# Optimization experiments

Measured on AMD Instinct MI355X. Metric: run time of the kernel, lower is better.

Reference implementation:

```python
import jax, jax.numpy as jnp
import numpy as np

B, S, HID = 2, 4096, 2048
NH, NKV, HD = 16, 4, 128  # num_heads, num_kv_heads, head_dim
GROUPS = NH // NKV
ROPE_THETA = 10000.0


def _rope_cos_sin(position_ids):
    # position_ids: [B, S] int
    inv_freq = 1.0 / (ROPE_THETA ** (jnp.arange(0, HD, 2, dtype=jnp.float32) / HD))  # [HD/2]
    freqs = position_ids.astype(jnp.float32)[..., None] * inv_freq  # [B, S, HD/2]
    emb = jnp.concatenate([freqs, freqs], axis=-1)  # [B, S, HD]
    return jnp.cos(emb), jnp.sin(emb)


def _rotate_half(x):
    x1, x2 = jnp.split(x, 2, axis=-1)
    return jnp.concatenate([-x2, x1], axis=-1)


def _apply_rope(q, k, cos, sin):
    # q: [B, NH, S, HD], k: [B, NKV, S, HD]; cos/sin: [B, S, HD]
    cos = cos[:, None, :, :]
    sin = sin[:, None, :, :]
    q = q * cos + _rotate_half(q) * sin
    k = k * cos + _rotate_half(k) * sin
    return q, k


def kappa(x):
    return jax.nn.elu(x) + 1.0


def setup_inputs() -> dict:
    key = jax.random.key(0)
    ks = jax.random.split(key, 8)
    sc = 0.02
    hidden_states = jax.random.normal(ks[0], (B, S, HID), dtype=jnp.float32)
    position_ids = jnp.broadcast_to(jnp.arange(S, dtype=jnp.int64)[None, :], (B, S))
    Wq = jax.random.normal(ks[1], (HID, NH * HD), dtype=jnp.float32) * sc
    Wk = jax.random.normal(ks[2], (HID, NKV * HD), dtype=jnp.float32) * sc
    Wv = jax.random.normal(ks[3], (HID, NKV * HD), dtype=jnp.float32) * sc
    Wo = jax.random.normal(ks[4], (HID, HID), dtype=jnp.float32) * sc
    Wphi = jax.random.normal(ks[5], (HID, HID), dtype=jnp.float32) * sc
    bphi = jax.random.normal(ks[6], (HID,), dtype=jnp.float32) * sc
    return {"hidden_states": hidden_states, "position_ids": position_ids,
            "Wq": Wq, "Wk": Wk, "Wv": Wv, "Wo": Wo, "Wphi": Wphi, "bphi": bphi}


def reference(hidden_states, position_ids, Wq, Wk, Wv, Wo, Wphi, bphi):
    b, s, _ = hidden_states.shape
    # projections -> [B, heads, S, HD]
    q = (hidden_states @ Wq).reshape(b, s, NH, HD).transpose(0, 2, 1, 3)
    k = (hidden_states @ Wk).reshape(b, s, NKV, HD).transpose(0, 2, 1, 3)
    v = (hidden_states @ Wv).reshape(b, s, NKV, HD).transpose(0, 2, 1, 3)
    cos, sin = _rope_cos_sin(position_ids)
    q, k = _apply_rope(q, k, cos, sin)
    # GQA expand kv heads
    k = jnp.repeat(k, GROUPS, axis=1)  # [B, NH, S, HD]
    v = jnp.repeat(v, GROUPS, axis=1)
    Qk = kappa(q)
    Kk = kappa(k)
    Qg = Qk.mean(axis=2)  # [B, NH, HD]
    logits = jnp.einsum('bnd,bnsd->bns', Qg, Kk)
    alpha = jax.nn.softmax(logits, axis=-1) * float(s)  # [B, NH, S]
    outer_sum = jnp.einsum('bns,bnsd,bnsf->bndf', alpha, Kk, v)  # [B, NH, HD, HD]
    X_phi = (hidden_states @ Wphi + bphi).reshape(b, s, NH, HD).transpose(0, 2, 1, 3)
    result_attn = jnp.einsum('bnsd,bndf->bnsf', Qk, outer_sum)
    context = (X_phi * result_attn).transpose(0, 2, 1, 3).reshape(b, s, HID)
    return context @ Wo
```

## Files before the change

kernel.cpp:

```cpp
#include <hip/hip_runtime.h>
#include <hip/hip_bf16.h>
#include <math.h>

#define B_    2
#define S_    4096
#define HID_  2048
#define NH_   16
#define NKV_  4
#define HD_   128
#define GROUPS_ (NH_/NKV_)
#define ROPE_THETA_ 10000.0f
#define OSPLIT 8
#define QCH   32

typedef __attribute__((ext_vector_type(8))) short short8;
typedef __attribute__((ext_vector_type(4))) float f32x4;

__device__ inline unsigned short f2bf(float f) {
    __hip_bfloat16 h = __float2bfloat16(f);
    return *(unsigned short*)&h;
}

__device__ inline float bf2f(short u) {
    union { unsigned int i; float f; } v;
    v.i = ((unsigned int)(unsigned short)u) << 16;
    return v.f;
}

__device__ inline void gload16(const void* g, void* l) {
    __builtin_amdgcn_global_load_lds((const __attribute__((address_space(1))) void*)g,
                                     (__attribute__((address_space(3))) void*)l, 16, 0, 0);
}

#define BARM() asm volatile("s_barrier" ::: "memory")

__global__ void rope_table_kernel(float* __restrict__ cosT, float* __restrict__ sinT) {
    int s = blockIdx.x;
    int i = threadIdx.x;
    float expo = -2.0f * (float)i / (float)HD_;
    float invf = powf(ROPE_THETA_, expo);
    float f = (float)s * invf;
    cosT[s * 64 + i] = cosf(f);
    sinT[s * 64 + i] = sinf(f);
}

__global__ void cast_bf16_kernel(const float* __restrict__ in,
                                 __hip_bfloat16* __restrict__ out, int n8) {
    int i = blockIdx.x * 256 + threadIdx.x;
    if (i >= n8) return;
    const float4 v0 = *reinterpret_cast<const float4*>(&in[i * 8]);
    const float4 v1 = *reinterpret_cast<const float4*>(&in[i * 8 + 4]);
    union { short8 v; unsigned short u[8]; } o;
    o.u[0] = f2bf(v0.x); o.u[1] = f2bf(v0.y); o.u[2] = f2bf(v0.z); o.u[3] = f2bf(v0.w);
    o.u[4] = f2bf(v1.x); o.u[5] = f2bf(v1.y); o.u[6] = f2bf(v1.z); o.u[7] = f2bf(v1.w);
    *reinterpret_cast<short8*>(&out[i * 8]) = o.v;
}

__global__ __launch_bounds__(256) void transpose_cast_kernel(
        const float* __restrict__ W, __hip_bfloat16* __restrict__ Wt, int K, int N) {
    __shared__ float T[64][65];
    int k0 = blockIdx.y * 64, n0 = blockIdx.x * 64;
    int tid = threadIdx.x;
    int r = tid >> 4, c4 = (tid & 15) * 4;
#pragma unroll
    for (int p = 0; p < 4; ++p) {
        float4 v = *reinterpret_cast<const float4*>(&W[(size_t)(k0 + r + p * 16) * N + n0 + c4]);
        T[r + p * 16][c4 + 0] = v.x;
        T[r + p * 16][c4 + 1] = v.y;
        T[r + p * 16][c4 + 2] = v.z;
        T[r + p * 16][c4 + 3] = v.w;
    }
    __syncthreads();
#pragma unroll
    for (int p = 0; p < 4; ++p) {
        int n = r + p * 16;
        short4 o;
        o.x = (short)f2bf(T[c4 + 0][n]);
        o.y = (short)f2bf(T[c4 + 1][n]);
        o.z = (short)f2bf(T[c4 + 2][n]);
        o.w = (short)f2bf(T[c4 + 3][n]);
        *reinterpret_cast<short4*>(&Wt[(size_t)(n0 + n) * K + k0 + c4]) = o;
    }
}

__device__ __forceinline__ void stage_region(const __hip_bfloat16* __restrict__ src,
        int ldK, int row0, int kbase, __hip_bfloat16* dst, int tid) {
#pragma unroll
    for (int g = 0; g < 2; ++g) {
        int P = g * 512 + tid;
        int row = P >> 2, cp = P & 3;
        int cl = cp ^ ((row >> 1) & 3);
        gload16(src + (size_t)(row0 + row) * ldK + kbase + cl * 8, dst + P * 8);
    }
}

__device__ __forceinline__ void stage_region128(const __hip_bfloat16* __restrict__ src,
        int ldK, int row0, int kbase, __hip_bfloat16* dst, int tid) {
#pragma unroll
    for (int g = 0; g < 2; ++g) {
        int P = g * 256 + tid;
        int row = P >> 2, cp = P & 3;
        int cl = cp ^ ((row >> 1) & 3);
        gload16(src + (size_t)(row0 + row) * ldK + kbase + cl * 8, dst + P * 8);
    }
}

#define BM 128
#define BN 128
#define T128EL 8192
__global__ __launch_bounds__(256) void gemm_mfma_kernel(
        const __hip_bfloat16* __restrict__ A, const __hip_bfloat16* __restrict__ Bt,
        float* __restrict__ C, const float* __restrict__ bias, int M, int N, int K) {
    __shared__ __hip_bfloat16 lds[4 * T128EL];
    int tid  = threadIdx.x;
    int wid  = tid >> 6, lane = tid & 63;
    int wr   = wid >> 1, wc = wid & 1;
    int lr = lane & 15, lc = lane >> 4;
    int c16 = lc ^ ((lr >> 1) & 3);
    int bm = blockIdx.y * BM, bn = blockIdx.x * BN;

    f32x4 acc[4][4];
#pragma unroll
    for (int m = 0; m < 4; ++m)
#pragma unroll
        for (int n = 0; n < 4; ++n)
#pragma unroll
            for (int i = 0; i < 4; ++i) acc[m][n][i] = 0.0f;

    const int NKT = K >> 5;

    stage_region128(A,  K, bm, 0,  lds,                 tid);
    stage_region128(Bt, K, bn, 0,  lds + 4096,          tid);
    stage_region128(A,  K, bm, 32, lds + T128EL,        tid);
    stage_region128(Bt, K, bn, 32, lds + T128EL + 4096, tid);
    asm volatile("s_waitcnt vmcnt(4)" ::: "memory");
    BARM();

    for (int kt = 0; kt < NKT; ++kt) {
        __hip_bfloat16* buf = lds + (size_t)(kt & 3) * T128EL;
        __hip_bfloat16* stg = lds + (size_t)((kt + 2) & 3) * T128EL;
        const bool pf = (kt + 2 < NKT);
        if (pf) {
            stage_region128(A,  K, bm, (kt + 2) << 5, stg,        tid);
            stage_region128(Bt, K, bn, (kt + 2) << 5, stg + 4096, tid);
        }
        short8 af[4], bf[4];
#pragma unroll
        for (int m = 0; m < 4; ++m)
            af[m] = *reinterpret_cast<const short8*>(
                &buf[(size_t)(wr * 64 + m * 16 + lr) * 32 + c16 * 8]);
#pragma unroll
        for (int n = 0; n < 4; ++n)
            bf[n] = *reinterpret_cast<const short8*>(
                &buf[4096 + (size_t)(wc * 64 + n * 16 + lr) * 32 + c16 * 8]);
        __builtin_amdgcn_s_setprio(1);
#pragma unroll
        for (int m = 0; m < 4; ++m)
#pragma unroll
            for (int n = 0; n < 4; ++n)
                acc[m][n] = __builtin_amdgcn_mfma_f32_16x16x32_bf16(
                    af[m], bf[n], acc[m][n], 0, 0, 0);
        __builtin_amdgcn_s_setprio(0);
        if (pf) { asm volatile("s_waitcnt vmcnt(4)" ::: "memory"); }
        else    { asm volatile("s_waitcnt vmcnt(0)" ::: "memory"); }
        BARM();
    }

    int lq = lane >> 4;
#pragma unroll
    for (int m = 0; m < 4; ++m) {
#pragma unroll
        for (int n = 0; n < 4; ++n) {
            int row = bm + wr * 64 + m * 16 + lq * 4;
            int col = bn + wc * 64 + n * 16 + lr;
            float bv = (bias != nullptr) ? bias[col] : 0.0f;
#pragma unroll
            for (int r = 0; r < 4; ++r)
                C[(size_t)(row + r) * N + col] = acc[m][n][r] + bv;
        }
    }
}

#define TBUFEL 16384

__global__ __launch_bounds__(512, 2) void gemm_mfma256_kernel(
        const __hip_bfloat16* __restrict__ A, const __hip_bfloat16* __restrict__ Bt,
        float* __restrict__ C, __hip_bfloat16* __restrict__ Cb,
        const float* __restrict__ bias, int M, int N, int K) {
    __shared__ __hip_bfloat16 lds[4 * TBUFEL];
    int tid = threadIdx.x, lane = tid & 63, wid = tid >> 6;
    int wr = wid >> 2, wc = wid & 3;
    int lr = lane & 15, lc = lane >> 4;
    int c16 = lc ^ ((lr >> 1) & 3);

    int nwg = gridDim.x;
    int orig = blockIdx.x;
    int q = nwg >> 3, r = nwg & 7;
    int xcd = orig & 7, lid = orig >> 3;
    int wg = (xcd < r ? xcd * (q + 1) : r * (q + 1) + (xcd - r) * q) + lid;
    int tiles_n = N >> 8;
    int bm = (wg / tiles_n) << 8, bn = (wg % tiles_n) << 8;

    f32x4 acc[8][4];
#pragma unroll
    for (int m = 0; m < 8; ++m)
#pragma unroll
        for (int n = 0; n < 4; ++n)
#pragma unroll
            for (int i = 0; i < 4; ++i) acc[m][n][i] = 0.0f;

    const int NKT = K >> 5;

    stage_region(A,  K, bm, 0,  lds,                 tid);
    stage_region(Bt, K, bn, 0,  lds + 8192,          tid);
    stage_region(A,  K, bm, 32, lds + TBUFEL,        tid);
    stage_region(Bt, K, bn, 32, lds + TBUFEL + 8192, tid);
    asm volatile("s_waitcnt vmcnt(4)" ::: "memory");
    BARM();

    for (int kt = 0; kt < NKT; ++kt) {
        __hip_bfloat16* buf = lds + (size_t)(kt & 3) * TBUFEL;
        __hip_bfloat16* stg = lds + (size_t)((kt + 2) & 3) * TBUFEL;
        const bool pf = (kt + 2 < NKT);

        if (pf) {
            stage_region(A,  K, bm, (kt + 2) << 5, stg,        tid);
            stage_region(Bt, K, bn, (kt + 2) << 5, stg + 8192, tid);
        }
        short8 b0[4], a0[4], a1[4];
#pragma unroll
        for (int n = 0; n < 4; ++n)
            b0[n] = *reinterpret_cast<const short8*>(
                &buf[8192 + (size_t)(wc * 64 + n * 16 + lr) * 32 + c16 * 8]);
#pragma unroll
        for (int m = 0; m < 4; ++m)
            a0[m] = *reinterpret_cast<const short8*>(
                &buf[(size_t)(wr * 128 + m * 16 + lr) * 32 + c16 * 8]);
        __builtin_amdgcn_s_setprio(1);
#pragma unroll
        for (int m = 0; m < 4; ++m)
#pragma unroll
            for (int n = 0; n < 4; ++n)
                acc[m][n] = __builtin_amdgcn_mfma_f32_16x16x32_bf16(
                    a0[m], b0[n], acc[m][n], 0, 0, 0);
        __builtin_amdgcn_s_setprio(0);
#pragma unroll
        for (int m = 0; m < 4; ++m)
            a1[m] = *reinterpret_cast<const short8*>(
                &buf[(size_t)(wr * 128 + 64 + m * 16 + lr) * 32 + c16 * 8]);
        __builtin_amdgcn_s_setprio(1);
#pragma unroll
        for (int m = 0; m < 4; ++m)
#pragma unroll
            for (int n = 0; n < 4; ++n)
                acc[m + 4][n] = __builtin_amdgcn_mfma_f32_16x16x32_bf16(
                    a1[m], b0[n], acc[m + 4][n], 0, 0, 0);
        __builtin_amdgcn_s_setprio(0);
        if (pf) { asm volatile("s_waitcnt vmcnt(4)" ::: "memory"); }
        else    { asm volatile("s_waitcnt vmcnt(0)" ::: "memory"); }
        BARM();
    }

    int lq = lane >> 4;
#pragma unroll
    for (int m = 0; m < 8; ++m) {
#pragma unroll
        for (int n = 0; n < 4; ++n) {
            int row = bm + wr * 128 + m * 16 + lq * 4;
            int col = bn + wc * 64 + n * 16 + lr;
            float bv = (bias != nullptr) ? bias[col] : 0.0f;
            if (Cb != nullptr) {
#pragma unroll
                for (int rr = 0; rr < 4; ++rr)
                    Cb[(size_t)(row + rr) * N + col] = __float2bfloat16(acc[m][n][rr] + bv);
            } else {
#pragma unroll
                for (int rr = 0; rr < 4; ++rr)
                    C[(size_t)(row + rr) * N + col] = acc[m][n][rr] + bv;
            }
        }
    }
}

__global__ void rope_kappa_q_kernel(__hip_bfloat16* __restrict__ Qb,
                                    const float* __restrict__ cosT,
                                    const float* __restrict__ sinT, int total) {
    int idx = blockIdx.x * 256 + threadIdx.x;
    if (idx >= total) return;
    int dq = idx & 15;
    int t  = idx >> 4;
    int n  = t % NH_;
    int bs = t / NH_;
    int s  = bs % S_;
    size_t base = (size_t)bs * (NH_ * HD_) + n * HD_ + dq * 4;
    short4 v1 = *reinterpret_cast<short4*>(&Qb[base]);
    short4 v2 = *reinterpret_cast<short4*>(&Qb[base + 64]);
    float4 c4 = *reinterpret_cast<const float4*>(&cosT[s * 64 + dq * 4]);
    float4 s4 = *reinterpret_cast<const float4*>(&sinT[s * 64 + dq * 4]);
    float x1[4] = {bf2f(v1.x), bf2f(v1.y), bf2f(v1.z), bf2f(v1.w)};
    float x2[4] = {bf2f(v2.x), bf2f(v2.y), bf2f(v2.z), bf2f(v2.w)};
    float cc[4] = {c4.x, c4.y, c4.z, c4.w};
    float ss[4] = {s4.x, s4.y, s4.z, s4.w};
    short4 o1, o2;
    short r1s[4], r2s[4];
#pragma unroll
    for (int j = 0; j < 4; ++j) {
        float r1 = x1[j] * cc[j] - x2[j] * ss[j];
        float r2 = x2[j] * cc[j] + x1[j] * ss[j];
        r1 = (r1 > 0.0f) ? (r1 + 1.0f) : expf(r1);
        r2 = (r2 > 0.0f) ? (r2 + 1.0f) : expf(r2);
        r1s[j] = (short)f2bf(r1);
        r2s[j] = (short)f2bf(r2);
    }
    o1.x = r1s[0]; o1.y = r1s[1]; o1.z = r1s[2]; o1.w = r1s[3];
    o2.x = r2s[0]; o2.y = r2s[1]; o2.z = r2s[2]; o2.w = r2s[3];
    *reinterpret_cast<short4*>(&Qb[base])      = o1;
    *reinterpret_cast<short4*>(&Qb[base + 64]) = o2;
}

__global__ void rope_kappa_kernel(float* __restrict__ X,
                                  const float* __restrict__ cosT,
                                  const float* __restrict__ sinT,
                                  int nheads, int rs, int total) {
    int idx = blockIdx.x * blockDim.x + threadIdx.x;
    if (idx >= total) return;
    int d  = idx & 63;
    int t  = idx >> 6;
    int n  = t % nheads;
    int bs = t / nheads;
    int s  = bs % S_;
    size_t base = (size_t)bs * rs + n * HD_;
    float c = cosT[s * 64 + d];
    float sn = sinT[s * 64 + d];
    float x1 = X[base + d];
    float x2 = X[base + d + 64];
    float r1 = x1 * c - x2 * sn;
    float r2 = x2 * c + x1 * sn;
    r1 = (r1 > 0.0f) ? (r1 + 1.0f) : expf(r1);
    r2 = (r2 > 0.0f) ? (r2 + 1.0f) : expf(r2);
    X[base + d] = r1;
    X[base + d + 64] = r2;
}

__global__ __launch_bounds__(256) void qg_partial_kernel(
        const __hip_bfloat16* __restrict__ Qb, float* __restrict__ QPART) {
    int blk = blockIdx.x;
    int c   = blk % QCH;
    int bn  = blk / QCH;
    int b = bn / NH_, n = bn % NH_;
    int t = threadIdx.x;
    int d8 = (t & 15) * 8;
    int sg = t >> 4;
    float acc[8] = {};
    int s0 = c * (S_ / QCH);
    for (int s = s0 + sg; s < s0 + S_ / QCH; s += 16) {
        short8 v = *reinterpret_cast<const short8*>(
            &Qb[((size_t)b * S_ + s) * (NH_ * HD_) + n * HD_ + d8]);
#pragma unroll
        for (int j = 0; j < 8; ++j) acc[j] += bf2f(v[j]);
    }
    __shared__ float red[16][128];
#pragma unroll
    for (int j = 0; j < 8; ++j) red[sg][d8 + j] = acc[j];
    __syncthreads();
    if (t < 128) {
        float s = 0.0f;
#pragma unroll
        for (int g = 0; g < 16; ++g) s += red[g][t];
        QPART[(size_t)(c * (B_ * NH_) + bn) * HD_ + t] = s;
    }
}

__global__ __launch_bounds__(256) void qg_reduce_kernel(
        const float* __restrict__ QPART, float* __restrict__ QG) {
    int idx = blockIdx.x * 256 + threadIdx.x;
    float acc = 0.0f;
#pragma unroll
    for (int c = 0; c < QCH; ++c)
        acc += QPART[(size_t)c * (B_ * NH_ * HD_) + idx];
    QG[idx] = acc * (1.0f / (float)S_);
}

__global__ __launch_bounds__(256) void logits_kernel(
        const float* __restrict__ KV, const float* __restrict__ QG,
        float* __restrict__ LG) {
    int bk = blockIdx.x;
    int b = bk / NKV_, kn = bk % NKV_;
    int s0 = blockIdx.y * 256;
    int w = threadIdx.x >> 6, lane = threadIdx.x & 63;
    float2 qv[GROUPS_];
#pragma unroll
    for (int g = 0; g < GROUPS_; ++g)
        qv[g] = *reinterpret_cast<const float2*>(
            &QG[(size_t)(b * NH_ + kn * GROUPS_ + g) * HD_ + lane * 2]);
    for (int i = 0; i < 64; ++i) {
        int s = s0 + w * 64 + i;
        float2 kv = *reinterpret_cast<const float2*>(
            &KV[((size_t)b * S_ + s) * 1024 + kn * HD_ + lane * 2]);
        float p[GROUPS_];
#pragma unroll
        for (int g = 0; g < GROUPS_; ++g) p[g] = kv.x * qv[g].x + kv.y * qv[g].y;
#pragma unroll
        for (int off = 32; off > 0; off >>= 1)
#pragma unroll
            for (int g = 0; g < GROUPS_; ++g) p[g] += __shfl_xor(p[g], off);
        if (lane == 0) {
#pragma unroll
            for (int g = 0; g < GROUPS_; ++g)
                LG[(size_t)(b * NH_ + kn * GROUPS_ + g) * S_ + s] = p[g];
        }
    }
}

__global__ __launch_bounds__(256) void softmax_alpha_kernel(float* __restrict__ LG) {
    int bn = blockIdx.x;
    float* row = &LG[(size_t)bn * S_];
    __shared__ float lg[S_];
    __shared__ float red[256];
    int tid = threadIdx.x;
    float lmax = -1e30f;
    for (int s = tid; s < S_; s += 256) {
        float v = row[s];
        lg[s] = v;
        lmax = fmaxf(lmax, v);
    }
    red[tid] = lmax;
    __syncthreads();
    for (int off = 128; off > 0; off >>= 1) {
        if (tid < off) red[tid] = fmaxf(red[tid], red[tid + off]);
        __syncthreads();
    }
    float mx = red[0];
    __syncthreads();
    float lsum = 0.0f;
    for (int s = tid; s < S_; s += 256) {
        float e = expf(lg[s] - mx);
        lg[s] = e;
        lsum += e;
    }
    red[tid] = lsum;
    __syncthreads();
    for (int off = 128; off > 0; off >>= 1) {
        if (tid < off) red[tid] += red[tid + off];
        __syncthreads();
    }
    float inv = (float)S_ / red[0];
    for (int s = tid; s < S_; s += 256)
        row[s] = lg[s] * inv;
}

__global__ __launch_bounds__(256) void kvt_kernel(
        const float* __restrict__ KV, const float* __restrict__ ALPHA,
        __hip_bfloat16* __restrict__ AKT, __hip_bfloat16* __restrict__ VT) {
    int bk = blockIdx.x;
    int b = bk / NKV_, kn = bk % NKV_;
    int s0 = blockIdx.y * 64;
    int isV = blockIdx.z;
    __shared__ float T[64][HD_ + 4];
    __shared__ float alf[GROUPS_][64];
    int tid = threadIdx.x;

    int r = tid >> 2;
    int c0 = (tid & 3) * 32;
    const float* src = KV + ((size_t)(b * S_) + s0 + r) * 1024 + isV * 512 + kn * HD_ + c0;
#pragma unroll
    for (int i = 0; i < 8; ++i)
        *reinterpret_cast<float4*>(&T[r][c0 + i * 4]) =
            *reinterpret_cast<const float4*>(src + i * 4);
    if (!isV) {
        int g = tid >> 6, ss = tid & 63;
        alf[g][ss] = ALPHA[(size_t)(b * NH_ + kn * GROUPS_ + g) * S_ + s0 + ss];
    }
    __syncthreads();

    int d  = tid >> 1;
    int sh = (tid & 1) * 32;
    if (isV) {
        __hip_bfloat16* dst = VT + ((size_t)bk * HD_ + d) * S_ + s0 + sh;
#pragma unroll
        for (int i = 0; i < 8; ++i) {
            short4 o;
            o.x = (short)f2bf(T[sh + i * 4 + 0][d]);
            o.y = (short)f2bf(T[sh + i * 4 + 1][d]);
            o.z = (short)f2bf(T[sh + i * 4 + 2][d]);
            o.w = (short)f2bf(T[sh + i * 4 + 3][d]);
            *reinterpret_cast<short4*>(dst + i * 4) = o;
        }
    } else {
#pragma unroll
        for (int g = 0; g < GROUPS_; ++g) {
            int n = kn * GROUPS_ + g;
            __hip_bfloat16* dst = AKT + ((size_t)(b * NH_ + n) * HD_ + d) * S_ + s0 + sh;
#pragma unroll
            for (int i = 0; i < 8; ++i) {
                short4 o;
                o.x = (short)f2bf(T[sh + i * 4 + 0][d] * alf[g][sh + i * 4 + 0]);
                o.y = (short)f2bf(T[sh + i * 4 + 1][d] * alf[g][sh + i * 4 + 1]);
                o.z = (short)f2bf(T[sh + i * 4 + 2][d] * alf[g][sh + i * 4 + 2]);
                o.w = (short)f2bf(T[sh + i * 4 + 3][d] * alf[g][sh + i * 4 + 3]);
                *reinterpret_cast<short4*>(dst + i * 4) = o;
            }
        }
    }
}

__global__ __launch_bounds__(256) void outer_mfma_kernel(
        const __hip_bfloat16* __restrict__ AKT, const __hip_bfloat16* __restrict__ VT,
        float* __restrict__ OPT) {
    int bn = blockIdx.x;
    int sp = blockIdx.y;
    int b = bn / NH_, n = bn % NH_;
    int kn = n / GROUPS_;
    const __hip_bfloat16* Abase = AKT + (size_t)bn * HD_ * S_ + sp * (S_ / OSPLIT);
    const __hip_bfloat16* Bbase = VT + (size_t)(b * NKV_ + kn) * HD_ * S_ + sp * (S_ / OSPLIT);
    __shared__ __hip_bfloat16 As[128 * 32];
    __shared__ __hip_bfloat16 Bs[128 * 32];
    int tid = threadIdx.x, lane = tid & 63, wid = tid >> 6;
    int wr = wid >> 1, wc = wid & 1;
    int lr = lane & 15, kq = (lane >> 4) * 8;

    f32x4 acc[4][4];
#pragma unroll
    for (int m = 0; m < 4; ++m)
#pragma unroll
        for (int nn = 0; nn < 4; ++nn)
#pragma unroll
            for (int i = 0; i < 4; ++i) acc[m][nn][i] = 0.0f;

    for (int ks = 0; ks < (S_ / OSPLIT) / 32; ++ks) {
        int k0 = ks * 32;
#pragma unroll
        for (int g = 0; g < 2; ++g) {
            int P = g * 256 + tid;
            int row = P >> 2, gr = P & 3;
            gload16(Abase + (size_t)row * S_ + k0 + gr * 8, As + P * 8);
            gload16(Bbase + (size_t)row * S_ + k0 + gr * 8, Bs + P * 8);
        }
        __syncthreads();
        short8 af[4], bf[4];
#pragma unroll
        for (int m = 0; m < 4; ++m)
            af[m] = *reinterpret_cast<short8*>(&As[(wr * 64 + m * 16 + lr) * 32 + kq]);
#pragma unroll
        for (int nn = 0; nn < 4; ++nn)
            bf[nn] = *reinterpret_cast<short8*>(&Bs[(wc * 64 + nn * 16 + lr) * 32 + kq]);
#pragma unroll
        for (int m = 0; m < 4; ++m)
#pragma unroll
            for (int nn = 0; nn < 4; ++nn)
                acc[m][nn] = __builtin_amdgcn_mfma_f32_16x16x32_bf16(
                    af[m], bf[nn], acc[m][nn], 0, 0, 0);
        __syncthreads();
    }

    float* base = OPT + ((size_t)bn * OSPLIT + sp) * (HD_ * HD_);
    int lq = lane >> 4;
#pragma unroll
    for (int m = 0; m < 4; ++m) {
#pragma unroll
        for (int nn = 0; nn < 4; ++nn) {
            int drow = wr * 64 + m * 16 + lq * 4;
            int fcol = wc * 64 + nn * 16 + lr;
            float4 o;
            o.x = acc[m][nn][0]; o.y = acc[m][nn][1];
            o.z = acc[m][nn][2]; o.w = acc[m][nn][3];
            *reinterpret_cast<float4*>(&base[(size_t)fcol * HD_ + drow]) = o;
        }
    }
}

__global__ __launch_bounds__(256) void outer_reduce_tc_kernel(
        const float* __restrict__ OPT, __hip_bfloat16* __restrict__ OUTt) {
    int idx = blockIdx.x * 256 + threadIdx.x;
    int bn = idx >> 11;
    int rem = idx & 2047;
    int f = rem >> 4, g = rem & 15;
    const float* src = OPT + (size_t)bn * OSPLIT * 16384 + f * 128 + g * 8;
    float s[8] = {};
#pragma unroll
    for (int sp = 0; sp < OSPLIT; ++sp) {
        float4 v0 = *reinterpret_cast<const float4*>(src + (size_t)sp * 16384);
        float4 v1 = *reinterpret_cast<const float4*>(src + (size_t)sp * 16384 + 4);
        s[0] += v0.x; s[1] += v0.y; s[2] += v0.z; s[3] += v0.w;
        s[4] += v1.x; s[5] += v1.y; s[6] += v1.z; s[7] += v1.w;
    }
    int gp = g ^ (f & 7);
    union { short8 v; unsigned short u[8]; } o;
#pragma unroll
    for (int j = 0; j < 8; ++j) o.u[j] = f2bf(s[j]);
    *reinterpret_cast<short8*>(&OUTt[(size_t)bn * 16384 + f * 128 + gp * 8]) = o.v;
}

__global__ __launch_bounds__(256) void attn_context_mfma_kernel(
        const __hip_bfloat16* __restrict__ Qb, const __hip_bfloat16* __restrict__ OUTt,
        const __hip_bfloat16* __restrict__ XPHIb, __hip_bfloat16* __restrict__ CTX) {
    int bn = blockIdx.x;
    int b = bn / NH_, n = bn % NH_;
    int s0 = blockIdx.y * 256;
    __shared__ __hip_bfloat16 Ms[128 * 128];
    int tid = threadIdx.x, lane = tid & 63, wid = tid >> 6;
    int lr = lane & 15, lc = lane >> 4;

#pragma unroll
    for (int g = 0; g < 8; ++g) {
        int P = g * 256 + tid;
        gload16(OUTt + (size_t)bn * 16384 + (size_t)P * 8, Ms + (size_t)P * 8);
    }

    f32x4 acc[4][8];
#pragma unroll
    for (int m = 0; m < 4; ++m)
#pragma unroll
        for (int nn = 0; nn < 8; ++nn)
#pragma unroll
            for (int i = 0; i < 4; ++i) acc[m][nn][i] = 0.0f;

    __syncthreads();

    const __hip_bfloat16* qbase =
        Qb + ((size_t)(b * S_) + s0 + wid * 64) * (NH_ * HD_) + n * HD_;
#pragma unroll
    for (int ks = 0; ks < 4; ++ks) {
        int k8 = ks * 32 + lc * 8;
        short8 a[4];
#pragma unroll
        for (int m = 0; m < 4; ++m)
            a[m] = *reinterpret_cast<const short8*>(
                qbase + (size_t)(m * 16 + lr) * (NH_ * HD_) + k8);
        int gfull = ks * 4 + lc;
        short8 bb[8];
#pragma unroll
        for (int nn = 0; nn < 8; ++nn) {
            int f = nn * 16 + lr;
            int gp = gfull ^ (f & 7);
            bb[nn] = *reinterpret_cast<const short8*>(&Ms[f * 128 + gp * 8]);
        }
#pragma unroll
        for (int m = 0; m < 4; ++m)
#pragma unroll
            for (int nn = 0; nn < 8; ++nn)
                acc[m][nn] = __builtin_amdgcn_mfma_f32_16x16x32_bf16(
                    a[m], bb[nn], acc[m][nn], 0, 0, 0);
    }

#pragma unroll
    for (int m = 0; m < 4; ++m) {
#pragma unroll
        for (int nn = 0; nn < 8; ++nn) {
            int row = s0 + wid * 64 + m * 16 + lc * 4;
            int f = nn * 16 + lr;
            size_t gi = ((size_t)(b * S_) + row) * (NH_ * HD_) + n * HD_ + f;
#pragma unroll
            for (int r = 0; r < 4; ++r) {
                float xp = __bfloat162float(XPHIb[gi + (size_t)r * (NH_ * HD_)]);
                CTX[gi + (size_t)r * (NH_ * HD_)] = __float2bfloat16(acc[m][nn][r] * xp);
            }
        }
    }
}

extern "C" void kernel_launch(void* const* d_in, const int* in_sizes, int n_in,
                              void* d_out, int out_size, void* d_ws, size_t ws_size,
                              hipStream_t stream) {
    (void)in_sizes; (void)n_in; (void)out_size; (void)ws_size;
    const float* X    = (const float*)d_in[0];
    const float* Wq   = (const float*)d_in[2];
    const float* Wk   = (const float*)d_in[3];
    const float* Wv   = (const float*)d_in[4];
    const float* Wo   = (const float*)d_in[5];
    const float* Wphi = (const float*)d_in[6];
    const float* bphi = (const float*)d_in[7];
    float* out = (float*)d_out;

    float* ws = (float*)d_ws;
    const size_t nQ = (size_t)B_ * S_ * NH_ * HD_;
    const size_t nK = (size_t)B_ * S_ * NKV_ * HD_;
    float* Q     = ws;
    float* KV    = Q + nQ;
    float* XPHI  = KV + 2 * nK;
    float* QG    = XPHI + nQ;
    float* ALPHA = QG + (size_t)B_ * NH_ * HD_;
    float* QPART = ALPHA + (size_t)B_ * NH_ * S_;
    float* COST  = QPART + (size_t)QCH * B_ * NH_ * HD_;
    float* SINT  = COST + (size_t)S_ * 64;
    __hip_bfloat16* Xb    = (__hip_bfloat16*)(SINT + (size_t)S_ * 64);
    __hip_bfloat16* Wqt   = Xb + nQ;
    __hip_bfloat16* Wkt   = Wqt + (size_t)HID_ * (NH_ * HD_);
    __hip_bfloat16* Wvt   = Wkt + (size_t)HID_ * (NKV_ * HD_);
    __hip_bfloat16* Wphit = Wvt + (size_t)HID_ * (NKV_ * HD_);
    __hip_bfloat16* Wot   = Wphit + (size_t)HID_ * (NH_ * HD_);
    __hip_bfloat16* OUTt  = Wot + (size_t)HID_ * HID_;
    __hip_bfloat16* VT    = OUTt + (size_t)B_ * NH_ * HD_ * HD_;
    float* OPT = (float*)(VT + nK);
    __hip_bfloat16* Qb    = (__hip_bfloat16*)Q;
    __hip_bfloat16* AKT   = Xb;
    __hip_bfloat16* XPHIb = (__hip_bfloat16*)XPHI;
    __hip_bfloat16* CTXb  = (__hip_bfloat16*)KV;

    const int M = B_ * S_;

    rope_table_kernel<<<S_, 64, 0, stream>>>(COST, SINT);
    cast_bf16_kernel<<<(int)(nQ / 8 / 256), 256, 0, stream>>>(X, Xb, (int)(nQ / 8));
    transpose_cast_kernel<<<dim3((NH_ * HD_) / 64, HID_ / 64), 256, 0, stream>>>(Wq, Wqt, HID_, NH_ * HD_);
    transpose_cast_kernel<<<dim3((NKV_ * HD_) / 64, HID_ / 64), 256, 0, stream>>>(Wk, Wkt, HID_, NKV_ * HD_);
    transpose_cast_kernel<<<dim3((NKV_ * HD_) / 64, HID_ / 64), 256, 0, stream>>>(Wv, Wvt, HID_, NKV_ * HD_);
    transpose_cast_kernel<<<dim3((NH_ * HD_) / 64, HID_ / 64), 256, 0, stream>>>(Wphi, Wphit, HID_, NH_ * HD_);
    transpose_cast_kernel<<<dim3(HID_ / 64, HID_ / 64), 256, 0, stream>>>(Wo, Wot, HID_, HID_);

    gemm_mfma256_kernel<<<(M / 256) * ((NH_ * HD_) / 256), 512, 0, stream>>>(
        Xb, Wqt, nullptr, Qb, nullptr, M, NH_ * HD_, HID_);
    gemm_mfma_kernel<<<dim3(1024 / BN, M / BM), 256, 0, stream>>>(
        Xb, Wkt, KV, nullptr, M, 1024, HID_);
    gemm_mfma256_kernel<<<(M / 256) * ((NH_ * HD_) / 256), 512, 0, stream>>>(
        Xb, Wphit, nullptr, XPHIb, bphi, M, NH_ * HD_, HID_);

    {
        int totalQ = B_ * S_ * NH_ * 16;
        rope_kappa_q_kernel<<<totalQ / 256, 256, 0, stream>>>(Qb, COST, SINT, totalQ);
        int totalK = B_ * S_ * NKV_ * 64;
        rope_kappa_kernel<<<totalK / 256, 256, 0, stream>>>(KV, COST, SINT, NKV_, 1024, totalK);
    }

    qg_partial_kernel<<<B_ * NH_ * QCH, 256, 0, stream>>>(Qb, QPART);
    qg_reduce_kernel<<<(B_ * NH_ * HD_) / 256, 256, 0, stream>>>(QPART, QG);
    logits_kernel<<<dim3(B_ * NKV_, S_ / 256), 256, 0, stream>>>(KV, QG, ALPHA);
    softmax_alpha_kernel<<<B_ * NH_, 256, 0, stream>>>(ALPHA);

    kvt_kernel<<<dim3(B_ * NKV_, S_ / 64, 2), 256, 0, stream>>>(KV, ALPHA, AKT, VT);
    outer_mfma_kernel<<<dim3(B_ * NH_, OSPLIT), 256, 0, stream>>>(AKT, VT, OPT);
    outer_reduce_tc_kernel<<<(B_ * NH_ * HD_ * 16) / 256, 256, 0, stream>>>(OPT, OUTt);

    attn_context_mfma_kernel<<<dim3(B_ * NH_, S_ / 256), 256, 0, stream>>>(
        Qb, OUTt, XPHIb, CTXb);

    gemm_mfma256_kernel<<<(M / 256) * (HID_ / 256), 512, 0, stream>>>(
        CTXb, Wot, out, nullptr, nullptr, M, HID_, HID_);
}
```

Before: 440.1 us.

## Restructure 256x256 GEMM to K=64 double-buffer with interleaved prefetch; widen softmax blocks

The large bf16 GEMM switches from a four-stage K=32 ring buffer to two K=64 buffers with an 8-slot XOR swizzle. Global loads for the next tile are split into pieces and issued between MFMA sub-blocks, with extra barriers around each phase. This aims to overlap loads with math better and halve the number of loop iterations, at the cost of more barriers per iteration and a tighter buffer-reuse schedule. The softmax kernel also moves from 256 to 1024 threads per block, to raise parallelism on a grid of only 32 blocks.

After: 430.1 us. 1.02x faster.

```diff
diff --git a/kernel.cpp b/kernel.cpp
--- a/kernel.cpp
+++ b/kernel.cpp
@@ -80,17 +80,6 @@
         o.z = (short)f2bf(T[c4 + 2][n]);
         o.w = (short)f2bf(T[c4 + 3][n]);
         *reinterpret_cast<short4*>(&Wt[(size_t)(n0 + n) * K + k0 + c4]) = o;
-    }
-}
-
-__device__ __forceinline__ void stage_region(const __hip_bfloat16* __restrict__ src,
-        int ldK, int row0, int kbase, __hip_bfloat16* dst, int tid) {
-#pragma unroll
-    for (int g = 0; g < 2; ++g) {
-        int P = g * 512 + tid;
-        int row = P >> 2, cp = P & 3;
-        int cl = cp ^ ((row >> 1) & 3);
-        gload16(src + (size_t)(row0 + row) * ldK + kbase + cl * 8, dst + P * 8);
     }
 }
 
@@ -181,17 +170,40 @@
     }
 }
 
-#define TBUFEL 16384
+#define HBUF 32768
+
+__device__ __forceinline__ void stageA64(const __hip_bfloat16* __restrict__ A,
+        int ldK, int bm, int k0, __hip_bfloat16* dst, int g, int tid) {
+    int P = g * 512 + tid;
+    int row = P >> 3, sp = P & 7;
+    gload16(A + (size_t)(bm + row) * ldK + k0 + ((sp ^ (row & 7)) << 3),
+            dst + (size_t)P * 8);
+}
+__device__ __forceinline__ void stageB64(const __hip_bfloat16* __restrict__ Bt,
+        int ldK, int bn, int k0, __hip_bfloat16* dst, int g, int tid) {
+    int P = g * 512 + tid;
+    int row = P >> 3, sp = P & 7;
+    gload16(Bt + (size_t)(bn + row) * ldK + k0 + ((sp ^ (row & 7)) << 3),
+            dst + 16384 + (size_t)P * 8);
+}
+
+__device__ __forceinline__ short8 ldsA64(const __hip_bfloat16* buf, int row, int slot_log) {
+    int sp = slot_log ^ (row & 7);
+    return *reinterpret_cast<const short8*>(&buf[(size_t)row * 64 + sp * 8]);
+}
+__device__ __forceinline__ short8 ldsB64(const __hip_bfloat16* buf, int row, int slot_log) {
+    int sp = slot_log ^ (row & 7);
+    return *reinterpret_cast<const short8*>(&buf[16384 + (size_t)row * 64 + sp * 8]);
+}
 
 __global__ __launch_bounds__(512, 2) void gemm_mfma256_kernel(
         const __hip_bfloat16* __restrict__ A, const __hip_bfloat16* __restrict__ Bt,
         float* __restrict__ C, __hip_bfloat16* __restrict__ Cb,
         const float* __restrict__ bias, int M, int N, int K) {
-    __shared__ __hip_bfloat16 lds[4 * TBUFEL];
+    __shared__ __hip_bfloat16 lds[2 * HBUF];
     int tid = threadIdx.x, lane = tid & 63, wid = tid >> 6;
     int wr = wid >> 2, wc = wid & 3;
     int lr = lane & 15, lc = lane >> 4;
-    int c16 = lc ^ ((lr >> 1) & 3);
 
     int nwg = gridDim.x;
     int orig = blockIdx.x;
@@ -209,56 +221,102 @@
 #pragma unroll
             for (int i = 0; i < 4; ++i) acc[m][n][i] = 0.0f;
 
-    const int NKT = K >> 5;
-
-    stage_region(A,  K, bm, 0,  lds,                 tid);
-    stage_region(Bt, K, bn, 0,  lds + 8192,          tid);
-    stage_region(A,  K, bm, 32, lds + TBUFEL,        tid);
-    stage_region(Bt, K, bn, 32, lds + TBUFEL + 8192, tid);
-    asm volatile("s_waitcnt vmcnt(4)" ::: "memory");
+    const int NKT = K >> 6;
+    __hip_bfloat16* buf0 = lds;
+    __hip_bfloat16* buf1 = lds + HBUF;
+
+#pragma unroll
+    for (int g = 0; g < 4; ++g) stageA64(A, K, bm, 0, buf0, g, tid);
+#pragma unroll
+    for (int g = 0; g < 4; ++g) stageB64(Bt, K, bn, 0, buf0, g, tid);
+    stageA64(A, K, bm, 64, buf1, 0, tid);
+    stageA64(A, K, bm, 64, buf1, 1, tid);
+    asm volatile("s_waitcnt vmcnt(2)" ::: "memory");
     BARM();
 
     for (int kt = 0; kt < NKT; ++kt) {
-        __hip_bfloat16* buf = lds + (size_t)(kt & 3) * TBUFEL;
-        __hip_bfloat16* stg = lds + (size_t)((kt + 2) & 3) * TBUFEL;
-        const bool pf = (kt + 2 < NKT);
-
-        if (pf) {
-            stage_region(A,  K, bm, (kt + 2) << 5, stg,        tid);
-            stage_region(Bt, K, bn, (kt + 2) << 5, stg + 8192, tid);
-        }
-        short8 b0[4], a0[4], a1[4];
-#pragma unroll
-        for (int n = 0; n < 4; ++n)
-            b0[n] = *reinterpret_cast<const short8*>(
-                &buf[8192 + (size_t)(wc * 64 + n * 16 + lr) * 32 + c16 * 8]);
-#pragma unroll
-        for (int m = 0; m < 4; ++m)
-            a0[m] = *reinterpret_cast<const short8*>(
-                &buf[(size_t)(wr * 128 + m * 16 + lr) * 32 + c16 * 8]);
-        __builtin_amdgcn_s_setprio(1);
-#pragma unroll
-        for (int m = 0; m < 4; ++m)
-#pragma unroll
-            for (int n = 0; n < 4; ++n)
-                acc[m][n] = __builtin_amdgcn_mfma_f32_16x16x32_bf16(
-                    a0[m], b0[n], acc[m][n], 0, 0, 0);
-        __builtin_amdgcn_s_setprio(0);
-#pragma unroll
-        for (int m = 0; m < 4; ++m)
-            a1[m] = *reinterpret_cast<const short8*>(
-                &buf[(size_t)(wr * 128 + 64 + m * 16 + lr) * 32 + c16 * 8]);
-        __builtin_amdgcn_s_setprio(1);
-#pragma unroll
-        for (int m = 0; m < 4; ++m)
-#pragma unroll
-            for (int n = 0; n < 4; ++n)
-                acc[m + 4][n] = __builtin_amdgcn_mfma_f32_16x16x32_bf16(
-                    a1[m], b0[n], acc[m + 4][n], 0, 0, 0);
-        __builtin_amdgcn_s_setprio(0);
-        if (pf) { asm volatile("s_waitcnt vmcnt(4)" ::: "memory"); }
-        else    { asm volatile("s_waitcnt vmcnt(0)" ::: "memory"); }
-        BARM();
+        __hip_bfloat16* buf = (kt & 1) ? buf1 : buf0;
+        __hip_bfloat16* nxt = (kt & 1) ? buf0 : buf1;
+        const bool p1 = (kt + 1 < NKT), p2 = (kt + 2 < NKT);
+        const int kn1 = (kt + 1) << 6;
+
+        short8 al[4], ah[4], bl[2], bh[2];
+
+#pragma unroll
+        for (int kk = 0; kk < 2; ++kk) {
+            int sl = kk * 4 + lc;
+#pragma unroll
+            for (int m = 0; m < 4; ++m)
+                al[m] = ldsA64(buf, wr * 128 + m * 16 + lr, sl);
+#pragma unroll
+            for (int n = 0; n < 2; ++n)
+                bl[n] = ldsB64(buf, wc * 64 + n * 16 + lr, sl);
+            if (kk == 0 && p1) {
+                stageA64(A, K, bm, kn1, nxt, 2, tid);
+                stageA64(A, K, bm, kn1, nxt, 3, tid);
+                stageB64(Bt, K, bn, kn1, nxt, 0, tid);
+            }
+            BARM();
+            __builtin_amdgcn_s_setprio(1);
+#pragma unroll
+            for (int m = 0; m < 4; ++m)
+#pragma unroll
+                for (int n = 0; n < 2; ++n)
+                    acc[m][n] = __builtin_amdgcn_mfma_f32_16x16x32_bf16(
+                        al[m], bl[n], acc[m][n], 0, 0, 0);
+            __builtin_amdgcn_s_setprio(0);
+            BARM();
+#pragma unroll
+            for (int m = 0; m < 4; ++m)
+                ah[m] = ldsA64(buf, wr * 128 + 64 + m * 16 + lr, sl);
+            if (kk == 0 && p1) {
+                stageB64(Bt, K, bn, kn1, nxt, 1, tid);
+                stageB64(Bt, K, bn, kn1, nxt, 2, tid);
+                stageB64(Bt, K, bn, kn1, nxt, 3, tid);
+            }
+            BARM();
+            __builtin_amdgcn_s_setprio(1);
+#pragma unroll
+            for (int m = 0; m < 4; ++m)
+#pragma unroll
+                for (int n = 0; n < 2; ++n)
+                    acc[m + 4][n] = __builtin_amdgcn_mfma_f32_16x16x32_bf16(
+                        ah[m], bl[n], acc[m + 4][n], 0, 0, 0);
+            __builtin_amdgcn_s_setprio(0);
+            BARM();
+#pragma unroll
+            for (int n = 0; n < 2; ++n)
+                bh[n] = ldsB64(buf, wc * 64 + (n + 2) * 16 + lr, sl);
+            BARM();
+            __builtin_amdgcn_s_setprio(1);
+#pragma unroll
+            for (int m = 0; m < 4; ++m)
+#pragma unroll
+                for (int n = 0; n < 2; ++n)
+                    acc[m][n + 2] = __builtin_amdgcn_mfma_f32_16x16x32_bf16(
+                        al[m], bh[n], acc[m][n + 2], 0, 0, 0);
+            __builtin_amdgcn_s_setprio(0);
+            BARM();
+            if (kk == 1 && p2) {
+                stageA64(A, K, bm, (kt + 2) << 6, buf, 0, tid);
+                stageA64(A, K, bm, (kt + 2) << 6, buf, 1, tid);
+            }
+            __builtin_amdgcn_s_setprio(1);
+#pragma unroll
+            for (int m = 0; m < 4; ++m)
+#pragma unroll
+                for (int n = 0; n < 2; ++n)
+                    acc[m + 4][n + 2] = __builtin_amdgcn_mfma_f32_16x16x32_bf16(
+                        ah[m], bh[n], acc[m + 4][n + 2], 0, 0, 0);
+            __builtin_amdgcn_s_setprio(0);
+            if (kk == 1) {
+                if (p2)      { asm volatile("s_waitcnt vmcnt(2)" ::: "memory"); }
+                else if (p1) { asm volatile("s_waitcnt vmcnt(0)" ::: "memory"); }
+                BARM();
+            } else {
+                BARM();
+            }
+        }
     }
 
     int lq = lane >> 4;
@@ -412,40 +470,40 @@
     }
 }
 
-__global__ __launch_bounds__(256) void softmax_alpha_kernel(float* __restrict__ LG) {
+__global__ __launch_bounds__(1024) void softmax_alpha_kernel(float* __restrict__ LG) {
     int bn = blockIdx.x;
     float* row = &LG[(size_t)bn * S_];
     __shared__ float lg[S_];
-    __shared__ float red[256];
+    __shared__ float red[1024];
     int tid = threadIdx.x;
     float lmax = -1e30f;
-    for (int s = tid; s < S_; s += 256) {
+    for (int s = tid; s < S_; s += 1024) {
         float v = row[s];
         lg[s] = v;
         lmax = fmaxf(lmax, v);
     }
     red[tid] = lmax;
     __syncthreads();
-    for (int off = 128; off > 0; off >>= 1) {
+    for (int off = 512; off > 0; off >>= 1) {
         if (tid < off) red[tid] = fmaxf(red[tid], red[tid + off]);
         __syncthreads();
     }
     float mx = red[0];
     __syncthreads();
     float lsum = 0.0f;
-    for (int s = tid; s < S_; s += 256) {
+    for (int s = tid; s < S_; s += 1024) {
         float e = expf(lg[s] - mx);
         lg[s] = e;
         lsum += e;
     }
     red[tid] = lsum;
     __syncthreads();
-    for (int off = 128; off > 0; off >>= 1) {
+    for (int off = 512; off > 0; off >>= 1) {
         if (tid < off) red[tid] += red[tid + off];
         __syncthreads();
     }
     float inv = (float)S_ / red[0];
-    for (int s = tid; s < S_; s += 256)
+    for (int s = tid; s < S_; s += 1024)
         row[s] = lg[s] * inv;
 }
 
@@ -724,7 +782,7 @@
     qg_partial_kernel<<<B_ * NH_ * QCH, 256, 0, stream>>>(Qb, QPART);
     qg_reduce_kernel<<<(B_ * NH_ * HD_) / 256, 256, 0, stream>>>(QPART, QG);
     logits_kernel<<<dim3(B_ * NKV_, S_ / 256), 256, 0, stream>>>(KV, QG, ALPHA);
-    softmax_alpha_kernel<<<B_ * NH_, 256, 0, stream>>>(ALPHA);
+    softmax_alpha_kernel<<<B_ * NH_, 1024, 0, stream>>>(ALPHA);
 
     kvt_kernel<<<dim3(B_ * NKV_, S_ / 64, 2), 256, 0, stream>>>(KV, ALPHA, AKT, VT);
     outer_mfma_kernel<<<dim3(B_ * NH_, OSPLIT), 256, 0, stream>>>(AKT, VT, OPT);
```
